# Performance work log

Hardware: AMD Instinct MI355X
Metric: run time of the kernel (lower is better)

## Reference

```python
import jax, jax.numpy as jnp
import numpy as np

N, E, IN_DIM, H, D = 100000, 1600000, 128, 4, 32


def setup_inputs() -> dict:
    key = jax.random.key(0)
    ks = jax.random.split(key, 8)
    glorot = lambda k, shape: jax.random.uniform(
        k, shape, jnp.float32, -1.0, 1.0) * np.sqrt(6.0 / (shape[0] + shape[1]))
    return {
        "x": jax.random.normal(ks[0], (N, IN_DIM), jnp.float32),
        "row": jax.random.randint(ks[1], (E,), 0, N, jnp.int32),
        "col": jax.random.randint(ks[2], (E,), 0, N, jnp.int32),
        "W_l": glorot(ks[3], (IN_DIM, H * D)),
        "W_r": glorot(ks[4], (IN_DIM, H * D)),
        "a1w": glorot(ks[5], (IN_DIM, H)),
        "a2w": glorot(ks[6], (IN_DIM, H)),
        "bias": jnp.zeros((H * D,), jnp.float32),
    }


def reference(x, row, col, W_l, W_r, a1w, a2w, bias):
    n = x.shape[0]  # num_nodes (= graph[0].max()+1 with dense random rows)
    x_l = (x @ W_l).reshape(n, H, D)          # [N,H,D]
    x_r = x @ W_r                              # [N,H*D]
    # per-edge attention logits: a1[row] + a2[col], leaky-relu(0.2)
    attn = jax.nn.leaky_relu((x @ a1w)[row] + (x @ a2w)[col], 0.2)  # [E,H]
    # segment softmax over destination rows (numerically stable)
    m = jax.ops.segment_max(attn, row, num_segments=n)               # [N,H]
    e = jnp.exp(attn - m[row])
    s = jax.ops.segment_sum(e, row, num_segments=n)                  # [N,H]
    attn_d = e / s[row]                                              # [E,H]
    # per-head SpMM: scatter-add weighted source features to destinations
    msgs = attn_d[:, :, None] * x_l[col]                             # [E,H,D]
    out = jax.ops.segment_sum(msgs, row, num_segments=n).reshape(n, H * D)
    return out + x_r + bias
```

## Files before the change

kernel.cpp:

```cpp
#include <hip/hip_runtime.h>


typedef short bfvec8 __attribute__((ext_vector_type(8)));
typedef float f32x4  __attribute__((ext_vector_type(4)));

#define BK 256
#define CAP 6144
#define EPB 4096
#define REC 256
#define BSTR 16

__device__ __forceinline__ unsigned short f2bf(float f) {
  union { float f; unsigned int i; } v; v.f = f;
  unsigned int r = v.i + 0x7fffu + ((v.i >> 16) & 1u);
  return (unsigned short)(r >> 16);
}

__global__ __launch_bounds__(128) void wprep_k(
    const float* __restrict__ Wl, const float* __restrict__ Wr,
    const float* __restrict__ a1w, const float* __restrict__ a2w,
    unsigned short* __restrict__ Wtg, int* __restrict__ bcur, int NBK)
{
  const int n = blockIdx.x;
  const int y = blockIdx.y;
  const int k = threadIdx.x;
  if (y == 0 && n < 4) {
    int b = n * 128 + k;
    if (b < NBK) bcur[b * BSTR] = b * CAP;
  }
  const float* W = y ? Wr : Wl;
  const float LOG2E = 1.4426950408889634f;
  float v;
  if (n < 128)      v = W[(size_t)k * 128 + n];
  else if (y)       v = 0.f;
  else if (n < 132) v = a1w[k * 4 + (n - 128)] * LOG2E;
  else              v = a2w[k * 4 + (n - 132)] * LOG2E;
  Wtg[((size_t)y * 136 + n) * 128 + k] = f2bf(v);
}

__global__ __launch_bounds__(256) void gemm_mfma(
    const float* __restrict__ x, const unsigned short* __restrict__ Wtg,
    const float* __restrict__ bias,
    char* __restrict__ xls, float* __restrict__ out,
    float* __restrict__ s1, float* __restrict__ s2, int N)
{
  __shared__ unsigned short xs[64][136];
  __shared__ unsigned short Ws[128][136];
  const int t = threadIdx.x;
  const int n0 = blockIdx.x * 64;

  for (int i = t; i < 2048; i += 256) {
    int rr = i >> 5, kc = (i & 31) << 2;
    float4 v = make_float4(0.f, 0.f, 0.f, 0.f);
    int n = n0 + rr;
    if (n < N) v = *(const float4*)&x[(size_t)n * 128 + kc];
    unsigned int lo = (unsigned int)f2bf(v.x) | ((unsigned int)f2bf(v.y) << 16);
    unsigned int hi = (unsigned int)f2bf(v.z) | ((unsigned int)f2bf(v.w) << 16);
    *(uint2*)&xs[rr][kc] = make_uint2(lo, hi);
  }

  const int w    = t >> 6;
  const int lane = t & 63;
  const int m    = lane & 15;
  const int quad = lane >> 4;

  bfvec8 afr[4];
  {
    int arow = 128 + (m < 8 ? m : 7);
    #pragma unroll
    for (int kc4 = 0; kc4 < 4; ++kc4)
      afr[kc4] = *(const bfvec8*)&Wtg[(size_t)arow * 128 + kc4 * 32 + quad * 8];
  }

  const int nrow = n0 + 16 * w + m;

  #pragma unroll
  for (int y = 0; y < 2; ++y) {
    const unsigned short* Wt = Wtg + (size_t)y * 136 * 128;
    if (y) __syncthreads();
    for (int i = t; i < 2048; i += 256) {
      int nr = i >> 4, kc = (i & 15) << 3;
      *(uint4*)&Ws[nr][kc] = *(const uint4*)&Wt[(size_t)nr * 128 + kc];
    }
    __syncthreads();

    f32x4 acc[9];
    #pragma unroll
    for (int i = 0; i < 9; ++i) acc[i] = (f32x4){0.f, 0.f, 0.f, 0.f};

    #pragma unroll
    for (int kc4 = 0; kc4 < 4; ++kc4) {
      const int kc = kc4 * 32;
      bfvec8 af = *(const bfvec8*)&xs[16 * w + m][kc + quad * 8];
      #pragma unroll
      for (int nt = 0; nt < 8; ++nt) {
        bfvec8 bfr = *(const bfvec8*)&Ws[nt * 16 + m][kc + quad * 8];
        acc[nt] = __builtin_amdgcn_mfma_f32_16x16x32_bf16(bfr, af, acc[nt], 0, 0, 0);
      }
      if (y == 0)
        acc[8] = __builtin_amdgcn_mfma_f32_16x16x32_bf16(afr[kc4], af, acc[8], 0, 0, 0);
    }

    if (nrow < N) {
      if (y) {
        #pragma unroll
        for (int nt = 0; nt < 8; ++nt) {
          int c = nt * 16 + quad * 4;
          float4 b4 = *(const float4*)&bias[c];
          float4 v = make_float4(acc[nt][0] + b4.x, acc[nt][1] + b4.y,
                                 acc[nt][2] + b4.z, acc[nt][3] + b4.w);
          *(float4*)&out[(size_t)nrow * 128 + c] = v;
        }
      } else {
        #pragma unroll
        for (int nt = 0; nt < 8; ++nt) {
          int c = nt * 16 + quad * 4;
          unsigned lo = (unsigned)f2bf(acc[nt][0]) | ((unsigned)f2bf(acc[nt][1]) << 16);
          unsigned hi = (unsigned)f2bf(acc[nt][2]) | ((unsigned)f2bf(acc[nt][3]) << 16);
          *(uint2*)(xls + ((size_t)nrow << 8) + 2 * c) = make_uint2(lo, hi);
        }
        if (quad == 0) *(f32x4*)&s1[nrow * 4] = acc[8];
        else if (quad == 1) *(f32x4*)&s2[nrow * 4] = acc[8];
      }
    }
  }
}

__global__ __launch_bounds__(256) void bin_k(const int* __restrict__ row,
    const int* __restrict__ col, int* __restrict__ bcur,
    unsigned int* __restrict__ binned, int E, int NBK)
{
  __shared__ int h[512];
  __shared__ int base[512];
  const int t = threadIdx.x;
  const int e0 = blockIdx.x * EPB;
  const int e1 = min(e0 + EPB, E);

  int rloc[16];
  for (int i = t; i < NBK; i += 256) h[i] = 0;
  __syncthreads();
  #pragma unroll
  for (int k = 0; k < 16; ++k) {
    int e = e0 + t + (k << 8);
    rloc[k] = (e < e1) ? row[e] : -1;
    if (rloc[k] >= 0) atomicAdd(&h[rloc[k] >> 8], 1);
  }
  __syncthreads();
  for (int i = t; i < NBK; i += 256) {
    int c = h[i];
    base[i] = c ? atomicAdd(&bcur[i * BSTR], c) : 0;
  }
  __syncthreads();
  for (int i = t; i < NBK; i += 256) h[i] = 0;
  __syncthreads();
  #pragma unroll
  for (int k = 0; k < 16; ++k) {
    int e = e0 + t + (k << 8);
    if (e < e1) {
      int r = rloc[k];
      unsigned c = (unsigned)col[e];
      int b = r >> 8;
      int rk = atomicAdd(&h[b], 1);
      binned[base[b] + rk] = ((unsigned)(r & 255) << 17) | c;
    }
  }
}

__global__ __launch_bounds__(256) void csr_k(const unsigned int* __restrict__ binned,
    const int* __restrict__ bcur, int* __restrict__ offs, int* __restrict__ deg,
    unsigned int* __restrict__ colsort, int N)
{
  __shared__ unsigned ecache[CAP];
  __shared__ int h[BK];
  __shared__ int sh[BK];
  const int t = threadIdx.x;
  const int b = blockIdx.x;
  const int lo = b * BK;
  const int e0 = b * CAP;
  const int e1 = bcur[b * BSTR];

  h[t] = 0;
  __syncthreads();
  for (int i = e0 + t; i < e1; i += 256) {
    unsigned p = binned[i];
    ecache[i - e0] = p;
    atomicAdd(&h[p >> 17], 1);
  }
  __syncthreads();

  int v = h[t];
  sh[t] = v;
  __syncthreads();
  for (int off = 1; off < 256; off <<= 1) {
    int tv = (t >= off) ? sh[t - off] : 0;
    __syncthreads();
    sh[t] += tv;
    __syncthreads();
  }
  int ex = sh[t] - v;
  int node = lo + t;
  if (node < N) { offs[node] = e0 + ex; deg[node] = v; }

  h[t] = ex;
  __syncthreads();
  const int cnt = e1 - e0;
  for (int i = t; i < cnt; i += 256) {
    unsigned p = ecache[i];
    int rlo = p >> 17;
    unsigned c = p & 0x1FFFFu;
    int pos = atomicAdd(&h[rlo], 1);
    colsort[e0 + pos] = c << 8;
  }
}

__global__ __launch_bounds__(256) void agg_k(const int* __restrict__ offs,
    const int* __restrict__ deg, const unsigned int* __restrict__ colsort,
    const float* __restrict__ s1, const float* __restrict__ s2,
    const char* __restrict__ xls, float* __restrict__ out, int N)
{
  const int lane = threadIdx.x & 63;
  const int n = blockIdx.x * 4 + (threadIdx.x >> 6);
  if (n >= N) return;
  const int e0 = offs[n], e1 = e0 + deg[n];
  const int h  = lane >> 4;
  const int hp = lane & 3;
  const int jj = (lane >> 2) & 7;
  const float s1c = s1[n * 4 + hp];
  const unsigned lane4 = (unsigned)(lane << 2);
  const unsigned hp4   = (unsigned)(hp << 2);
  const char* s2b = (const char*)s2;

  float acc0 = 0.f, acc1 = 0.f, wsum = 0.f;
  int i0 = e0;
  for (; i0 + 8 <= e1; i0 += 8) {
    unsigned csl = colsort[i0 + jj];
    float z2 = *(const float*)(s2b + ((csl >> 4) + hp4));
    float z = s1c + z2;
    z = fmaxf(z, 0.2f * z);
    float wv = exp2f(z);

    unsigned cs[8];
    #pragma unroll
    for (int j = 0; j < 8; ++j) cs[j] = colsort[i0 + j];
    unsigned pv[8];
    #pragma unroll
    for (int j = 0; j < 8; ++j)
      pv[j] = *(const unsigned*)(xls + (cs[j] + lane4));

    #pragma unroll
    for (int j = 0; j < 8; ++j) {
      float wj = __shfl(wv, (j << 2) | h);
      wsum += wj;
      union { unsigned u; float f; } lo, hi;
      lo.u = pv[j] << 16;
      hi.u = pv[j] & 0xffff0000u;
      acc0 += wj * lo.f;
      acc1 += wj * hi.f;
    }
  }
  if (i0 < e1) {
    const int rem = e1 - i0;
    unsigned csl = colsort[i0 + (jj < rem ? jj : rem - 1)];
    float z2 = *(const float*)(s2b + ((csl >> 4) + hp4));
    float z = s1c + z2;
    z = fmaxf(z, 0.2f * z);
    float wv = (jj < rem) ? exp2f(z) : 0.f;

    unsigned cs[8];
    #pragma unroll
    for (int j = 0; j < 8; ++j) cs[j] = colsort[i0 + (j < rem ? j : rem - 1)];
    unsigned pv[8];
    #pragma unroll
    for (int j = 0; j < 8; ++j)
      pv[j] = *(const unsigned*)(xls + (cs[j] + lane4));

    #pragma unroll
    for (int j = 0; j < 8; ++j) {
      float wj = __shfl(wv, (j << 2) | h);
      wsum += wj;
      union { unsigned u; float f; } lo, hi;
      lo.u = pv[j] << 16;
      hi.u = pv[j] & 0xffff0000u;
      acc0 += wj * lo.f;
      acc1 += wj * hi.f;
    }
  }

  float inv = (wsum > 0.f) ? (1.0f / wsum) : 0.f;
  const size_t o = (size_t)n * 128 + 2 * lane;
  float2 xr = *(const float2*)&out[o];
  float2 res; res.x = acc0 * inv + xr.x; res.y = acc1 * inv + xr.y;
  *(float2*)&out[o] = res;
}

extern "C" void kernel_launch(void* const* d_in, const int* in_sizes, int n_in,
                              void* d_out, int out_size, void* d_ws, size_t ws_size,
                              hipStream_t stream) {
  const float* x    = (const float*)d_in[0];
  const int*   row  = (const int*)d_in[1];
  const int*   col  = (const int*)d_in[2];
  const float* Wl   = (const float*)d_in[3];
  const float* Wr   = (const float*)d_in[4];
  const float* a1w  = (const float*)d_in[5];
  const float* a2w  = (const float*)d_in[6];
  const float* bias = (const float*)d_in[7];
  float* out = (float*)d_out;
  const int N = in_sizes[0] / 128;
  const int E = in_sizes[1];
  (void)n_in; (void)out_size; (void)ws_size;

  const int NBK = (N + BK - 1) / BK;

  char* ws = (char*)d_ws;
  size_t off = 0;
  auto carve = [&](size_t bytes) { void* p = ws + off; off += (bytes + 255) & ~(size_t)255; return p; };
  char* xls            = (char*)carve((size_t)N * REC);
  float* s1            = (float*)carve((size_t)N * 4 * 4);
  float* s2            = (float*)carve((size_t)N * 4 * 4);
  int* offs            = (int*)carve((size_t)N * 4);
  int* deg             = (int*)carve((size_t)N * 4);
  unsigned int* colsort= (unsigned int*)carve((size_t)NBK * CAP * 4);
  unsigned int* binned = (unsigned int*)carve((size_t)NBK * CAP * 4);
  int* bcur            = (int*)carve((size_t)NBK * BSTR * 4);
  unsigned short* Wtg  = (unsigned short*)carve((size_t)2 * 136 * 128 * 2);

  wprep_k  <<<dim3(136, 2), 128, 0, stream>>>(Wl, Wr, a1w, a2w, Wtg, bcur, NBK);
  gemm_mfma<<<(N + 63) / 64, 256, 0, stream>>>(x, Wtg, bias, xls, out, s1, s2, N);
  bin_k    <<<(E + EPB - 1) / EPB, 256, 0, stream>>>(row, col, bcur, binned, E, NBK);
  csr_k    <<<NBK, 256, 0, stream>>>(binned, bcur, offs, deg, colsort, N);
  agg_k    <<<(N + 3) / 4, 256, 0, stream>>>(offs, deg, colsort, s1, s2, xls, out, N);
}
```

Baseline: 277.3 us.

## Fuse edge binning into GEMM kernel with interleaved blocks and halve bucket size

Merges the edge-binning kernel into the GEMM launch by giving every third block the binning role, so the memory-bound binning and the MFMA GEMM run concurrently in one grid. Bucket size drops from 256 to 128 nodes, with smaller per-bucket capacity and 2048 edges per binning block. The CSR kernel is adjusted so only 128 threads take part in the per-bucket scan. This removes one launch and aims for better overlap and occupancy, but shared memory is sized for the GEMM path in all blocks, and the smaller bucket capacity leaves less headroom for overflow with skewed degrees.

```diff
diff --git a/kernel.cpp b/kernel.cpp
--- a/kernel.cpp
+++ b/kernel.cpp
@@ -4,9 +4,9 @@
 typedef short bfvec8 __attribute__((ext_vector_type(8)));
 typedef float f32x4  __attribute__((ext_vector_type(4)));
 
-#define BK 256
-#define CAP 6144
-#define EPB 4096
+#define BK 128
+#define CAPC 3584
+#define EPB 2048
 #define REC 256
 #define BSTR 16
 
@@ -24,9 +24,9 @@
   const int n = blockIdx.x;
   const int y = blockIdx.y;
   const int k = threadIdx.x;
-  if (y == 0 && n < 4) {
+  if (y == 0 && n < 8) {
     int b = n * 128 + k;
-    if (b < NBK) bcur[b * BSTR] = b * CAP;
+    if (b < NBK) bcur[b * BSTR] = b * CAPC;
   }
   const float* W = y ? Wr : Wl;
   const float LOG2E = 1.4426950408889634f;
@@ -38,16 +38,63 @@
   Wtg[((size_t)y * 136 + n) * 128 + k] = f2bf(v);
 }
 
-__global__ __launch_bounds__(256) void gemm_mfma(
+__global__ __launch_bounds__(256) void gemm_bin_k(
     const float* __restrict__ x, const unsigned short* __restrict__ Wtg,
     const float* __restrict__ bias,
     char* __restrict__ xls, float* __restrict__ out,
-    float* __restrict__ s1, float* __restrict__ s2, int N)
+    float* __restrict__ s1, float* __restrict__ s2, int N,
+    const int* __restrict__ row, const int* __restrict__ col,
+    int* __restrict__ bcur, unsigned int* __restrict__ binned,
+    int E, int NBK, int binBlocks, int gemmBlocks)
 {
-  __shared__ unsigned short xs[64][136];
-  __shared__ unsigned short Ws[128][136];
+  __shared__ __align__(16) char raw[52224];
+  const int bid = blockIdx.x;
   const int t = threadIdx.x;
-  const int n0 = blockIdx.x * 64;
+  const bool isbin = (bid % 3 == 0) && (bid / 3 < binBlocks);
+
+  if (isbin) {
+    int* h    = (int*)raw;
+    int* base = (int*)(raw + 4096);
+    const int sub = bid / 3;
+    const int e0 = sub * EPB;
+    const int e1 = min(e0 + EPB, E);
+
+    int rloc[8];
+    for (int i = t; i < NBK; i += 256) h[i] = 0;
+    __syncthreads();
+    #pragma unroll
+    for (int k = 0; k < 8; ++k) {
+      int e = e0 + t + (k << 8);
+      rloc[k] = (e < e1) ? row[e] : -1;
+      if (rloc[k] >= 0) atomicAdd(&h[rloc[k] >> 7], 1);
+    }
+    __syncthreads();
+    for (int i = t; i < NBK; i += 256) {
+      int c = h[i];
+      base[i] = c ? atomicAdd(&bcur[i * BSTR], c) : 0;
+    }
+    __syncthreads();
+    for (int i = t; i < NBK; i += 256) h[i] = 0;
+    __syncthreads();
+    #pragma unroll
+    for (int k = 0; k < 8; ++k) {
+      int e = e0 + t + (k << 8);
+      if (e < e1) {
+        int r = rloc[k];
+        unsigned c = (unsigned)col[e];
+        int b = r >> 7;
+        int rk = atomicAdd(&h[b], 1);
+        binned[base[b] + rk] = ((unsigned)(r & 127) << 17) | c;
+      }
+    }
+    return;
+  }
+
+  unsigned short (*xs)[136] = (unsigned short(*)[136])raw;
+  unsigned short (*Ws)[136] = (unsigned short(*)[136])(raw + 64*272);
+  const int sub = bid - min(bid / 3 + 1, binBlocks);
+  if (sub >= gemmBlocks) return;
+  const int n0 = sub * 64;
 
   for (int i = t; i < 2048; i += 256) {
     int rr = i >> 5, kc = (i & 31) << 2;
@@ -126,60 +173,20 @@
   }
 }
 
-__global__ __launch_bounds__(256) void bin_k(const int* __restrict__ row,
-    const int* __restrict__ col, int* __restrict__ bcur,
-    unsigned int* __restrict__ binned, int E, int NBK)
-{
-  __shared__ int h[512];
-  __shared__ int base[512];
-  const int t = threadIdx.x;
-  const int e0 = blockIdx.x * EPB;
-  const int e1 = min(e0 + EPB, E);
-
-  int rloc[16];
-  for (int i = t; i < NBK; i += 256) h[i] = 0;
-  __syncthreads();
-  #pragma unroll
-  for (int k = 0; k < 16; ++k) {
-    int e = e0 + t + (k << 8);
-    rloc[k] = (e < e1) ? row[e] : -1;
-    if (rloc[k] >= 0) atomicAdd(&h[rloc[k] >> 8], 1);
-  }
-  __syncthreads();
-  for (int i = t; i < NBK; i += 256) {
-    int c = h[i];
-    base[i] = c ? atomicAdd(&bcur[i * BSTR], c) : 0;
-  }
-  __syncthreads();
-  for (int i = t; i < NBK; i += 256) h[i] = 0;
-  __syncthreads();
-  #pragma unroll
-  for (int k = 0; k < 16; ++k) {
-    int e = e0 + t + (k << 8);
-    if (e < e1) {
-      int r = rloc[k];
-      unsigned c = (unsigned)col[e];
-      int b = r >> 8;
-      int rk = atomicAdd(&h[b], 1);
-      binned[base[b] + rk] = ((unsigned)(r & 255) << 17) | c;
-    }
-  }
-}
-
 __global__ __launch_bounds__(256) void csr_k(const unsigned int* __restrict__ binned,
     const int* __restrict__ bcur, int* __restrict__ offs, int* __restrict__ deg,
     unsigned int* __restrict__ colsort, int N)
 {
-  __shared__ unsigned ecache[CAP];
+  __shared__ unsigned ecache[CAPC];
   __shared__ int h[BK];
   __shared__ int sh[BK];
   const int t = threadIdx.x;
   const int b = blockIdx.x;
   const int lo = b * BK;
-  const int e0 = b * CAP;
+  const int e0 = b * CAPC;
   const int e1 = bcur[b * BSTR];
 
-  h[t] = 0;
+  if (t < BK) h[t] = 0;
   __syncthreads();
   for (int i = e0 + t; i < e1; i += 256) {
     unsigned p = binned[i];
@@ -188,20 +195,21 @@
   }
   __syncthreads();
 
-  int v = h[t];
-  sh[t] = v;
+  int v = 0;
+  if (t < BK) { v = h[t]; sh[t] = v; }
   __syncthreads();
-  for (int off = 1; off < 256; off <<= 1) {
-    int tv = (t >= off) ? sh[t - off] : 0;
-    __syncthreads();
-    sh[t] += tv;
-    __syncthreads();
-  }
-  int ex = sh[t] - v;
-  int node = lo + t;
-  if (node < N) { offs[node] = e0 + ex; deg[node] = v; }
-
-  h[t] = ex;
+  for (int off = 1; off < BK; off <<= 1) {
+    int tv = (t < BK && t >= off) ? sh[t - off] : 0;
+    __syncthreads();
+    if (t < BK) sh[t] += tv;
+    __syncthreads();
+  }
+  if (t < BK) {
+    int ex = sh[t] - v;
+    int node = lo + t;
+    if (node < N) { offs[node] = e0 + ex; deg[node] = v; }
+    h[t] = ex;
+  }
   __syncthreads();
   const int cnt = e1 - e0;
   for (int i = t; i < cnt; i += 256) {
@@ -319,14 +327,19 @@
   float* s2            = (float*)carve((size_t)N * 4 * 4);
   int* offs            = (int*)carve((size_t)N * 4);
   int* deg             = (int*)carve((size_t)N * 4);
-  unsigned int* colsort= (unsigned int*)carve((size_t)NBK * CAP * 4);
-  unsigned int* binned = (unsigned int*)carve((size_t)NBK * CAP * 4);
+  unsigned int* colsort= (unsigned int*)carve((size_t)NBK * CAPC * 4);
+  unsigned int* binned = (unsigned int*)carve((size_t)NBK * CAPC * 4);
   int* bcur            = (int*)carve((size_t)NBK * BSTR * 4);
   unsigned short* Wtg  = (unsigned short*)carve((size_t)2 * 136 * 128 * 2);
 
-  wprep_k  <<<dim3(136, 2), 128, 0, stream>>>(Wl, Wr, a1w, a2w, Wtg, bcur, NBK);
-  gemm_mfma<<<(N + 63) / 64, 256, 0, stream>>>(x, Wtg, bias, xls, out, s1, s2, N);
-  bin_k    <<<(E + EPB - 1) / EPB, 256, 0, stream>>>(row, col, bcur, binned, E, NBK);
-  csr_k    <<<NBK, 256, 0, stream>>>(binned, bcur, offs, deg, colsort, N);
-  agg_k    <<<(N + 3) / 4, 256, 0, stream>>>(offs, deg, colsort, s1, s2, xls, out, N);
-}
+  const int gemmBlocks = (N + 63) / 64;
+  const int binBlocks  = (E + EPB - 1) / EPB;
+  const int T = gemmBlocks + binBlocks;
+
+  wprep_k   <<<dim3(136, 2), 128, 0, stream>>>(Wl, Wr, a1w, a2w, Wtg, bcur, NBK);
+  gemm_bin_k<<<T, 256, 0, stream>>>(x, Wtg, bias, xls, out, s1, s2, N,
+                                    row, col, bcur, binned, E, NBK,
+                                    binBlocks, gemmBlocks);
+  csr_k     <<<NBK, 256, 0, stream>>>(binned, bcur, offs, deg, colsort, N);
+  agg_k     <<<(N + 3) / 4, 256, 0, stream>>>(offs, deg, colsort, s1, s2, xls, out, N);
+}
```

Result: faster. 269.7 us (-2.7%).
